# Kernel tuning notes

Measured on AMD Instinct MI355X. Metric: run time of the kernel, lower is better.

## Reference

```python
import jax, jax.numpy as jnp
import numpy as np

SL, BS, HS, FFN, E, TOPK = 2048, 4, 1024, 4096, 8, 2
T = SL * BS

def setup_inputs() -> dict:
    key = jax.random.key(0)
    k1, k2, k3, k4, k5, k6 = jax.random.split(key, 6)
    x = jax.random.normal(k1, (SL, BS, HS), dtype=jnp.float32)
    expert_weights = jax.random.uniform(k2, (T, TOPK), dtype=jnp.float32)
    expert_indices = jax.random.randint(k3, (T, TOPK), 0, E).astype(jnp.int64)
    scores = jax.random.uniform(k4, (T, TOPK), dtype=jnp.float32)
    w1 = jax.random.normal(k5, (E, HS, FFN), dtype=jnp.float32) * 0.02
    w2 = jax.random.normal(k6, (E, FFN, HS), dtype=jnp.float32) * 0.02
    return {"x": x, "expert_weights": expert_weights, "scores": scores,
            "w1": w1, "w2": w2, "expert_indices": expert_indices}

def reference(x, expert_weights, scores, w1, w2, expert_indices):
    # Dropless MoE dispatch-compute-combine with router_type=None.
    # Math identity: megablocks gather/grouped-GEMM/scatter with per-copy
    # expert_weights equals, for each token t:
    #   out[t] = sum_k expert_weights[t,k] * MLP_{e(t,k)}(x[t])
    # We fold the top-k copies into a per-(token, expert) combine weight and
    # run one GEMM pair per expert (fixed small E), matching the grouped GEMM.
    sl, bs, hs = x.shape
    num_experts = w1.shape[0]
    xf = x.reshape(-1, hs)  # [T, hs]
    onehot = jax.nn.one_hot(expert_indices, num_experts, dtype=x.dtype)  # [T, k, E]
    combine = jnp.einsum("tk,tke->et", expert_weights, onehot)  # [E, T]

    def expert_step(acc, inputs):
        w1e, w2e, cw = inputs  # [hs, ffn], [ffn, hs], [T]
        h = jax.nn.gelu(xf @ w1e, approximate=False)  # [T, ffn]
        acc = acc + cw[:, None] * (h @ w2e)  # [T, hs]
        return acc, None

    out, _ = jax.lax.scan(expert_step, jnp.zeros_like(xf), (w1, w2, combine))
    return out.reshape(sl, bs, hs)
```

## Files before the change

### kernel.cpp

```cpp
#include <hip/hip_runtime.h>
#include <hip/hip_bf16.h>
#include <math.h>
#include <stdint.h>

#define N_TOK   8192
#define HS      1024
#define FFN     4096
#define NE      8
#define NA      16384
#define CAP     16384
#define BMT     128
#define MAXT    136
#define PERMSZ  16777216ULL

typedef __attribute__((ext_vector_type(8))) short          bf16x8;
typedef __attribute__((ext_vector_type(4))) float          f32x4;
typedef __attribute__((ext_vector_type(4))) float          fvec4;
typedef __attribute__((ext_vector_type(4))) unsigned short usvec4;

__device__ __forceinline__ void gl_lds16(const void* g, void* l) {
  __builtin_amdgcn_global_load_lds(
      (const __attribute__((address_space(1))) unsigned int*)g,
      (__attribute__((address_space(3))) unsigned int*)l,
      16, 0, 0);
}

__device__ __forceinline__ unsigned short f2bf(float f) {
  union { float f; unsigned int u; } v; v.f = f;
  unsigned int r = v.u + 0x7FFFu + ((v.u >> 16) & 1u);
  return (unsigned short)(r >> 16);
}


__global__ void cvt_x_kernel(const fvec4* __restrict__ in, unsigned short* __restrict__ out, int n4) {
  int i = blockIdx.x * 256 + threadIdx.x;
  if (i >= n4) return;
  fvec4 v = in[i];
  usvec4 o;
  o[0] = f2bf(v[0]); o[1] = f2bf(v[1]); o[2] = f2bf(v[2]); o[3] = f2bf(v[3]);
  *(usvec4*)(out + (size_t)i * 4) = o;
}

__global__ void tpose_cvt_kernel(const float* __restrict__ in, unsigned short* __restrict__ out,
                                 int R, int C) {
  __shared__ float t[64][65];
  int bc = blockIdx.x * 64, br = blockIdx.y * 64, e = blockIdx.z;
  const float* ine = in + (size_t)e * R * C;
  unsigned short* oute = out + (size_t)e * R * C;
  int tx = threadIdx.x & 63, ty = threadIdx.x >> 6;
#pragma unroll
  for (int q = 0; q < 16; ++q) {
    int r = ty * 16 + q;
    t[r][tx] = ine[(size_t)(br + r) * C + bc + tx];
  }
  __syncthreads();
#pragma unroll
  for (int q = 0; q < 16; ++q) {
    int c = ty * 16 + q;
    oute[(size_t)(bc + c) * R + br + tx] = f2bf(t[tx][c]);
  }
}


__global__ void route_kernel(const int* __restrict__ idx, const float* __restrict__ wts,
                             int* __restrict__ counts, int* __restrict__ btok,
                             int* __restrict__ bslot, float* __restrict__ bw) {
  int a = blockIdx.x * 256 + threadIdx.x;
  if (a >= NA) return;
  int e = idx[a];
  int pos = atomicAdd(&counts[e], 1);
  btok[(size_t)e * CAP + pos]  = a >> 1;
  bslot[(size_t)e * CAP + pos] = a;
  bw[(size_t)e * CAP + pos]    = wts[a];
}

__global__ void build_tiles_kernel(int* __restrict__ counts, int2* __restrict__ table) {
  if (threadIdx.x == 0 && blockIdx.x == 0) {
    int nt = 0;
    for (int e = 0; e < NE; ++e) {
      int c = counts[e];
      int t = (c + BMT - 1) >> 7;
      for (int m = 0; m < t && nt < MAXT; ++m) table[nt++] = make_int2(e, m);
    }
    counts[8] = nt;
  }
}

template <int EPI, int AROW, int KTOT, int NU>
__global__ __launch_bounds__(256, 3)
void moe_gemm(const unsigned short* __restrict__ Ab,
              const unsigned short* __restrict__ Bb,
              unsigned short* __restrict__ hout,
              float* __restrict__ perm,
              const int* __restrict__ btok,
              const int* __restrict__ bslot,
              const float* __restrict__ bw,
              const int* __restrict__ counts,
              const int2* __restrict__ table,
              int* __restrict__ ctr, int p0, int tc) {
  constexpr int NT = KTOT / 32;
  __shared__ char lds[32768];
  __shared__ int s_u;

  int tid = threadIdx.x;
  int wid = tid >> 6, lane = tid & 63;
  int wm = wid >> 1, wn = wid & 1;
  int nt = counts[8];

  int rin = lane >> 2;
  int klog = ((lane & 3) * 16) ^ (((rin >> 1) & 3) << 4);
  int dst[4];
#pragma unroll
  for (int q = 0; q < 4; ++q) dst[q] = (wid * 4 + q) * 1024;

  int l15 = lane & 15, l16 = lane >> 4;
  int swzr = ((l15 >> 1) & 3) << 4;
  int ks = l16 * 16;
  int offA0 = (wm * 64 + l15) * 64 + (ks ^ swzr);
  int offB0 = 8192 + (wn * 64 + l15) * 64 + (ks ^ swzr);

  for (;;) {
    __syncthreads();
    if (tid == 0) s_u = atomicAdd(ctr, 1);
    __syncthreads();
    int u = s_u;
    if (u >= NU) return;

    int kq, col, j;
    if (EPI == 0) { kq = 0; col = u / MAXT; j = u % MAXT; }
    else          { kq = u / (8 * MAXT); int rem = u % (8 * MAXT); col = rem / MAXT; j = rem % MAXT; }
    if (j >= nt || j < p0 || j >= p0 + tc) continue;
    int2 te = table[j];
    int e = te.x, tm = te.y;
    int count = counts[e];
    int slotb = j - p0;
    int bn0 = col * 128;
    int kbyte0 = kq * (KTOT * 2);

    const unsigned short* Be = Bb + (size_t)e * ((size_t)FFN * HS);

    const char* src[4];
#pragma unroll
    for (int q = 0; q < 4; ++q) {
      int c = wid * 4 + q;
      if (c < 8) {
        int row = c * 16 + rin;
        if (EPI == 0) {
          int grow = tm * BMT + row;
          int tok = (grow < count) ? btok[(size_t)e * CAP + grow] : 0;
          src[q] = (const char*)(Ab + (size_t)tok * AROW) + kbyte0 + klog;
        } else {
          src[q] = (const char*)(Ab + ((size_t)slotb * BMT + row) * AROW) + kbyte0 + klog;
        }
      } else {
        int nrow = bn0 + (c - 8) * 16 + rin;
        src[q] = (const char*)(Be + (size_t)nrow * AROW) + kbyte0 + klog;
      }
    }

    f32x4 acc[4][4] = {};

#pragma unroll
    for (int q = 0; q < 4; ++q) gl_lds16(src[q], lds + dst[q]);
    asm volatile("s_waitcnt vmcnt(0)" ::: "memory");
    __builtin_amdgcn_s_barrier();
    __builtin_amdgcn_sched_barrier(0);

    for (int t = 0; t < NT; ++t) {
      const char* rbuf = lds + (t & 1) * 16384;
      char* db = lds + ((t + 1) & 1) * 16384;
      if (t + 1 < NT) {
#pragma unroll
        for (int q = 0; q < 4; ++q)
          gl_lds16(src[q] + (size_t)(t + 1) * 64, db + dst[q]);
      }
      bf16x8 a[4], b[4];
#pragma unroll
      for (int n = 0; n < 4; ++n) b[n] = *(const bf16x8*)(rbuf + offB0 + n * 1024);
#pragma unroll
      for (int i = 0; i < 4; ++i) a[i] = *(const bf16x8*)(rbuf + offA0 + i * 1024);
      __builtin_amdgcn_s_setprio(1);
#pragma unroll
      for (int i = 0; i < 4; ++i)
#pragma unroll
        for (int n = 0; n < 4; ++n)
          acc[i][n] = __builtin_amdgcn_mfma_f32_16x16x32_bf16(a[i], b[n], acc[i][n], 0, 0, 0);
      __builtin_amdgcn_s_setprio(0);
      __builtin_amdgcn_sched_barrier(0);
      asm volatile("s_waitcnt vmcnt(0)" ::: "memory");
      __builtin_amdgcn_s_barrier();
      __builtin_amdgcn_sched_barrier(0);
    }

    char* wlds = lds + wid * 8192;
#pragma unroll
    for (int p = 0; p < 2; ++p) {
#pragma unroll
      for (int ii = 0; ii < 2; ++ii) {
        int i = p * 2 + ii;
#pragma unroll
        for (int n = 0; n < 4; ++n) {
          int waddr = (ii * 16 + l16 * 4) * 256 + (n * 16 + l15) * 4;
#pragma unroll
          for (int rr = 0; rr < 4; ++rr)
            *(float*)(wlds + waddr + rr * 256) = acc[i][n][rr];
        }
      }
      asm volatile("s_waitcnt lgkmcnt(0)" ::: "memory");
      __builtin_amdgcn_sched_barrier(0);
#pragma unroll
      for (int rd = 0; rd < 8; ++rd) {
        int row = rd * 4 + l16;
        f32x4 v = *(const f32x4*)(wlds + row * 256 + l15 * 16);
        int colg = bn0 + wn * 64 + l15 * 4;
        if (EPI == 0) {
          usvec4 o;
#pragma unroll
          for (int z = 0; z < 4; ++z) {
            float vv = v[z];
            float x2 = vv * vv;
            float u2 = 1.5957691216057308f * vv * fmaf(0.044715f, x2, 1.0f);
            u2 = fminf(fmaxf(u2, -30.f), 30.f);
            float ee = __expf(u2);
            o[z] = f2bf(vv * __fdividef(ee, ee + 1.0f));
          }
          size_t hrow = (size_t)slotb * BMT + wm * 64 + p * 32 + row;
          *(usvec4*)(hout + hrow * FFN + colg) = o;
        } else {
          int grow = tm * BMT + wm * 64 + p * 32 + row;
          if (grow < count) {
            int s = bslot[(size_t)e * CAP + grow];
            float wgt = bw[(size_t)e * CAP + grow];
            fvec4 o;
#pragma unroll
            for (int z = 0; z < 4; ++z) o[z] = wgt * v[z];
            *(fvec4*)(perm + (size_t)kq * PERMSZ + (size_t)s * HS + colg) = o;
          }
        }
      }
      __builtin_amdgcn_sched_barrier(0);
    }
  }
}

__global__ void combine_kernel(const fvec4* __restrict__ perm, fvec4* __restrict__ out, int n4) {
  int i = blockIdx.x * 256 + threadIdx.x;
  if (i >= n4) return;
  int t = i >> 8;
  int c = i & 255;
  const fvec4* p0 = perm;
  const fvec4* p1 = perm + PERMSZ / 4;
  size_t r0 = (size_t)(2 * t) * 256 + c;
  size_t r1 = (size_t)(2 * t + 1) * 256 + c;
  out[i] = (p0[r0] + p1[r0]) + (p0[r1] + p1[r1]);
}


extern "C" void kernel_launch(void* const* d_in, const int* in_sizes, int n_in,
                              void* d_out, int out_size, void* d_ws, size_t ws_size,
                              hipStream_t stream) {
  const float* x   = (const float*)d_in[0];
  const float* ew  = (const float*)d_in[1];
  const float* w1  = (const float*)d_in[3];
  const float* w2  = (const float*)d_in[4];
  const int*   eix = (const int*)d_in[5];

  char* ws = (char*)d_ws;
  const size_t o_w1T    = 0;
  const size_t o_w2T    = 67108864ULL;
  const size_t o_xb     = 134217728ULL;
  const size_t o_btok   = 150994944ULL;
  const size_t o_bslot  = 151519232ULL;
  const size_t o_bw     = 152043520ULL;
  const size_t o_counts = 152567808ULL;
  const size_t o_table  = 152568064ULL;
  const size_t o_ctr    = 152570112ULL;
  const size_t o_perm   = 152572160ULL;
  const size_t o_h      = 286789888ULL;

  unsigned short* w1T = (unsigned short*)(ws + o_w1T);
  unsigned short* w2T = (unsigned short*)(ws + o_w2T);
  unsigned short* xb  = (unsigned short*)(ws + o_xb);
  int*   btok   = (int*)(ws + o_btok);
  int*   bslot  = (int*)(ws + o_bslot);
  float* bw     = (float*)(ws + o_bw);
  int*   counts = (int*)(ws + o_counts);
  int2*  table  = (int2*)(ws + o_table);
  int*   ctrs   = (int*)(ws + o_ctr);
  float* perm   = (float*)(ws + o_perm);
  unsigned short* hbuf = (unsigned short*)(ws + o_h);

  long long havail = (long long)ws_size - (long long)o_h;
  long long tile_bytes = (long long)BMT * FFN * 2;
  int tc = (int)(havail / tile_bytes);
  if (tc < 1) tc = 1;
  if (tc > MAXT) tc = MAXT;
  int npass = (MAXT + tc - 1) / tc;
  if (npass > 128) npass = 128;

  hipMemsetAsync(counts, 0, 256, stream);
  hipMemsetAsync(ctrs, 0, 2048, stream);

  cvt_x_kernel<<<(N_TOK * HS / 4 + 255) / 256, 256, 0, stream>>>(
      (const fvec4*)x, xb, N_TOK * HS / 4);
  tpose_cvt_kernel<<<dim3(FFN / 64, HS / 64, NE), 256, 0, stream>>>(w1, w1T, HS, FFN);
  tpose_cvt_kernel<<<dim3(HS / 64, FFN / 64, NE), 256, 0, stream>>>(w2, w2T, FFN, HS);

  route_kernel<<<(NA + 255) / 256, 256, 0, stream>>>(eix, ew, counts, btok, bslot, bw);
  build_tiles_kernel<<<1, 64, 0, stream>>>(counts, table);

  for (int p = 0; p < npass; ++p) {
    moe_gemm<0, HS, HS, 32 * MAXT><<<dim3(1024), 256, 0, stream>>>(
        xb, w1T, hbuf, perm, btok, bslot, bw, counts, table,
        &ctrs[p * 2 + 0], p * tc, tc);
    moe_gemm<1, FFN, FFN / 2, 2 * 8 * MAXT><<<dim3(1024), 256, 0, stream>>>(
        hbuf, w2T, hbuf, perm, btok, bslot, bw, counts, table,
        &ctrs[p * 2 + 1], p * tc, tc);
  }

  combine_kernel<<<(N_TOK * HS / 4 + 255) / 256, 256, 0, stream>>>(
      (const fvec4*)perm, (fvec4*)d_out, N_TOK * HS / 4);
}
```

Baseline: 684.1 us.

## Use 256x256 GEMM tiles with pre-packed swizzled operands and 4-stage LDS pipeline

Doubles the M tile to 256 rows and the N tile to 256 columns with 512-thread blocks and 128KB of LDS. The weights, the gathered tokens and the hidden activations are stored in a pre-tiled, swizzled bf16 layout, so each operand chunk is one contiguous 16KB block. Token gathering and conversion move into a separate pack kernel that runs after routing. The K loop becomes a 4-buffer ring with 3 stages in flight, replacing the previous double buffer with a full vmcnt(0) drain every step. This aims to raise operand reuse and hide memory latency, at the cost of 1 block per CU, more padding waste per expert from 256-row tiles, and a larger workspace.

Result: slower. 795.4 us (+16.3%).

```diff
diff --git a/kernel.cpp b/kernel.cpp
--- a/kernel.cpp
+++ b/kernel.cpp
@@ -9,14 +9,15 @@
 #define NE      8
 #define NA      16384
 #define CAP     16384
-#define BMT     128
-#define MAXT    136
+#define BMT     256
+#define MAXT    72
 #define PERMSZ  16777216ULL
 
 typedef __attribute__((ext_vector_type(8))) short          bf16x8;
 typedef __attribute__((ext_vector_type(4))) float          f32x4;
 typedef __attribute__((ext_vector_type(4))) float          fvec4;
 typedef __attribute__((ext_vector_type(4))) unsigned short usvec4;
+typedef __attribute__((ext_vector_type(8))) unsigned short usvec8;
 
 __device__ __forceinline__ void gl_lds16(const void* g, void* l) {
   __builtin_amdgcn_global_load_lds(
@@ -29,36 +30,6 @@
   union { float f; unsigned int u; } v; v.f = f;
   unsigned int r = v.u + 0x7FFFu + ((v.u >> 16) & 1u);
   return (unsigned short)(r >> 16);
-}
-
-
-__global__ void cvt_x_kernel(const fvec4* __restrict__ in, unsigned short* __restrict__ out, int n4) {
-  int i = blockIdx.x * 256 + threadIdx.x;
-  if (i >= n4) return;
-  fvec4 v = in[i];
-  usvec4 o;
-  o[0] = f2bf(v[0]); o[1] = f2bf(v[1]); o[2] = f2bf(v[2]); o[3] = f2bf(v[3]);
-  *(usvec4*)(out + (size_t)i * 4) = o;
-}
-
-__global__ void tpose_cvt_kernel(const float* __restrict__ in, unsigned short* __restrict__ out,
-                                 int R, int C) {
-  __shared__ float t[64][65];
-  int bc = blockIdx.x * 64, br = blockIdx.y * 64, e = blockIdx.z;
-  const float* ine = in + (size_t)e * R * C;
-  unsigned short* oute = out + (size_t)e * R * C;
-  int tx = threadIdx.x & 63, ty = threadIdx.x >> 6;
-#pragma unroll
-  for (int q = 0; q < 16; ++q) {
-    int r = ty * 16 + q;
-    t[r][tx] = ine[(size_t)(br + r) * C + bc + tx];
-  }
-  __syncthreads();
-#pragma unroll
-  for (int q = 0; q < 16; ++q) {
-    int c = ty * 16 + q;
-    oute[(size_t)(bc + c) * R + br + tx] = f2bf(t[tx][c]);
-  }
 }
 
 
@@ -79,122 +50,163 @@
     int nt = 0;
     for (int e = 0; e < NE; ++e) {
       int c = counts[e];
-      int t = (c + BMT - 1) >> 7;
+      int t = (c + BMT - 1) >> 8;
       for (int m = 0; m < t && nt < MAXT; ++m) table[nt++] = make_int2(e, m);
     }
     counts[8] = nt;
   }
 }
 
-template <int EPI, int AROW, int KTOT, int NU>
-__global__ __launch_bounds__(256, 3)
-void moe_gemm(const unsigned short* __restrict__ Ab,
-              const unsigned short* __restrict__ Bb,
+
+__global__ void pack_x_kernel(const float* __restrict__ x,
+                              unsigned short* __restrict__ xg,
+                              const int* __restrict__ btok,
+                              const int* __restrict__ counts,
+                              const int2* __restrict__ table) {
+  int j = blockIdx.x, kt = blockIdx.y, row = threadIdx.x;
+  int nt = counts[8];
+  if (j >= nt) return;
+  int2 te = table[j];
+  int e = te.x, tm = te.y;
+  int count = counts[e];
+  int grow = tm * BMT + row;
+  int tok = (grow < count) ? btok[(size_t)e * CAP + grow] : 0;
+  const fvec4* src = (const fvec4*)(x + (size_t)tok * HS + kt * 32);
+  char* dst = (char*)xg + ((size_t)j * 32 + kt) * 16384 + row * 64;
+  int swz = (row >> 1) & 3;
+#pragma unroll
+  for (int s = 0; s < 4; ++s) {
+    fvec4 v0 = src[2 * s], v1 = src[2 * s + 1];
+    usvec8 o;
+    o[0] = f2bf(v0[0]); o[1] = f2bf(v0[1]); o[2] = f2bf(v0[2]); o[3] = f2bf(v0[3]);
+    o[4] = f2bf(v1[0]); o[5] = f2bf(v1[1]); o[6] = f2bf(v1[2]); o[7] = f2bf(v1[3]);
+    *(usvec8*)(dst + ((s ^ swz) << 4)) = o;
+  }
+}
+
+__global__ void pack_w_kernel(const float* __restrict__ in, unsigned short* __restrict__ out,
+                              int R, int C) {
+  __shared__ float t[64][65];
+  int bc = blockIdx.x * 64, br = blockIdx.y * 64, e = blockIdx.z;
+  const float* ine = in + (size_t)e * R * C;
+  char* oute = (char*)out + (size_t)e * R * C * 2;
+  int tx = threadIdx.x & 63, ty = threadIdx.x >> 6;
+#pragma unroll
+  for (int q = 0; q < 16; ++q) {
+    int r = ty * 16 + q;
+    t[r][tx] = ine[(size_t)(br + r) * C + bc + tx];
+  }
+  __syncthreads();
+  int nkt = R / 32;
+#pragma unroll
+  for (int q = 0; q < 16; ++q) {
+    int c = ty * 16 + q;
+    int n = bc + c, k = br + tx;
+    size_t addr = (((size_t)(n >> 8) * nkt + (k >> 5)) * 256 + (n & 255)) * 64
+                + ((size_t)((((k & 31) >> 3) ^ ((n >> 1) & 3)) << 4)) + (k & 7) * 2;
+    *(unsigned short*)(oute + addr) = f2bf(t[tx][c]);
+  }
+}
+
+template <int EPI, int NKT, int NUNIT>
+__global__ __launch_bounds__(512, 1)
+void moe_gemm(const unsigned short* __restrict__ Apk,
+              const unsigned short* __restrict__ Bpk,
               unsigned short* __restrict__ hout,
               float* __restrict__ perm,
-              const int* __restrict__ btok,
               const int* __restrict__ bslot,
               const float* __restrict__ bw,
               const int* __restrict__ counts,
               const int2* __restrict__ table,
               int* __restrict__ ctr, int p0, int tc) {
-  constexpr int NT = KTOT / 32;
-  __shared__ char lds[32768];
+  __shared__ char lds[131072];
   __shared__ int s_u;
 
-  int tid = threadIdx.x;
-  int wid = tid >> 6, lane = tid & 63;
-  int wm = wid >> 1, wn = wid & 1;
+  int tid = threadIdx.x, wid = tid >> 6, lane = tid & 63;
+  int wm = wid >> 2, wn = wid & 3;
+  int l15 = lane & 15, l16 = lane >> 4;
   int nt = counts[8];
 
-  int rin = lane >> 2;
-  int klog = ((lane & 3) * 16) ^ (((rin >> 1) & 3) << 4);
-  int dst[4];
-#pragma unroll
-  for (int q = 0; q < 4; ++q) dst[q] = (wid * 4 + q) * 1024;
-
-  int l15 = lane & 15, l16 = lane >> 4;
-  int swzr = ((l15 >> 1) & 3) << 4;
-  int ks = l16 * 16;
-  int offA0 = (wm * 64 + l15) * 64 + (ks ^ swzr);
-  int offB0 = 8192 + (wn * 64 + l15) * 64 + (ks ^ swzr);
+  int swz16 = (l16 ^ ((l15 >> 1) & 3)) << 4;
+  int offA0 = (wm * 128 + l15) * 64 + swz16;
+  int offB0 = 16384 + (wn * 64 + l15) * 64 + swz16;
+  int cbase[4];
+#pragma unroll
+  for (int q = 0; q < 4; ++q) cbase[q] = (wid * 4 + q) * 1024;
 
   for (;;) {
     __syncthreads();
     if (tid == 0) s_u = atomicAdd(ctr, 1);
     __syncthreads();
     int u = s_u;
-    if (u >= NU) return;
-
-    int kq, col, j;
-    if (EPI == 0) { kq = 0; col = u / MAXT; j = u % MAXT; }
-    else          { kq = u / (8 * MAXT); int rem = u % (8 * MAXT); col = rem / MAXT; j = rem % MAXT; }
+    if (u >= NUNIT) return;
+
+    int j, col, kq;
+    if (EPI == 0) { col = u / MAXT; j = u - col * MAXT; kq = 0; }
+    else { int g = u / MAXT; j = u - g * MAXT; col = g & 3; kq = g >> 2; }
     if (j >= nt || j < p0 || j >= p0 + tc) continue;
     int2 te = table[j];
     int e = te.x, tm = te.y;
     int count = counts[e];
     int slotb = j - p0;
-    int bn0 = col * 128;
-    int kbyte0 = kq * (KTOT * 2);
-
-    const unsigned short* Be = Bb + (size_t)e * ((size_t)FFN * HS);
-
-    const char* src[4];
+
+    const char* Asrc; const char* Bsrc;
+    if (EPI == 0) {
+      Asrc = (const char*)Apk + (size_t)j * (32 * 16384);
+      Bsrc = (const char*)Bpk + (size_t)e * 8388608 + (size_t)col * (32 * 16384);
+    } else {
+      Asrc = (const char*)Apk + (size_t)slotb * (128 * 16384) + (size_t)kq * (64 * 16384);
+      Bsrc = (const char*)Bpk + (size_t)e * 8388608 + (size_t)col * (128 * 16384)
+           + (size_t)kq * (64 * 16384);
+    }
+    const char* csrc[4];
 #pragma unroll
     for (int q = 0; q < 4; ++q) {
       int c = wid * 4 + q;
-      if (c < 8) {
-        int row = c * 16 + rin;
-        if (EPI == 0) {
-          int grow = tm * BMT + row;
-          int tok = (grow < count) ? btok[(size_t)e * CAP + grow] : 0;
-          src[q] = (const char*)(Ab + (size_t)tok * AROW) + kbyte0 + klog;
-        } else {
-          src[q] = (const char*)(Ab + ((size_t)slotb * BMT + row) * AROW) + kbyte0 + klog;
-        }
-      } else {
-        int nrow = bn0 + (c - 8) * 16 + rin;
-        src[q] = (const char*)(Be + (size_t)nrow * AROW) + kbyte0 + klog;
-      }
-    }
-
-    f32x4 acc[4][4] = {};
-
-#pragma unroll
-    for (int q = 0; q < 4; ++q) gl_lds16(src[q], lds + dst[q]);
-    asm volatile("s_waitcnt vmcnt(0)" ::: "memory");
-    __builtin_amdgcn_s_barrier();
-    __builtin_amdgcn_sched_barrier(0);
-
-    for (int t = 0; t < NT; ++t) {
-      const char* rbuf = lds + (t & 1) * 16384;
-      char* db = lds + ((t + 1) & 1) * 16384;
-      if (t + 1 < NT) {
-#pragma unroll
-        for (int q = 0; q < 4; ++q)
-          gl_lds16(src[q] + (size_t)(t + 1) * 64, db + dst[q]);
-      }
-      bf16x8 a[4], b[4];
+      csrc[q] = (c < 16 ? Asrc + c * 1024 : Bsrc + (c - 16) * 1024) + lane * 16;
+    }
+
+    f32x4 acc[8][4] = {};
+
+#pragma unroll
+    for (int s = 0; s < 3; ++s)
+#pragma unroll
+      for (int q = 0; q < 4; ++q)
+        gl_lds16(csrc[q] + (size_t)s * 16384, lds + s * 32768 + cbase[q]);
+
+    for (int hk = 0; hk < NKT; ++hk) {
+      asm volatile("s_waitcnt vmcnt(8)" ::: "memory");
+      __builtin_amdgcn_sched_barrier(0);
+      __builtin_amdgcn_s_barrier();
+      __builtin_amdgcn_sched_barrier(0);
+
+      int hs = hk + 3; if (hs >= NKT) hs -= NKT;
+      char* db = lds + (hs & 3) * 32768;
+#pragma unroll
+      for (int q = 0; q < 4; ++q)
+        gl_lds16(csrc[q] + (size_t)hs * 16384, db + cbase[q]);
+
+      const char* rbuf = lds + (hk & 3) * 32768;
+      bf16x8 a[8], b[4];
 #pragma unroll
       for (int n = 0; n < 4; ++n) b[n] = *(const bf16x8*)(rbuf + offB0 + n * 1024);
 #pragma unroll
-      for (int i = 0; i < 4; ++i) a[i] = *(const bf16x8*)(rbuf + offA0 + i * 1024);
+      for (int i = 0; i < 8; ++i) a[i] = *(const bf16x8*)(rbuf + offA0 + i * 1024);
       __builtin_amdgcn_s_setprio(1);
 #pragma unroll
-      for (int i = 0; i < 4; ++i)
+      for (int i = 0; i < 8; ++i)
 #pragma unroll
         for (int n = 0; n < 4; ++n)
           acc[i][n] = __builtin_amdgcn_mfma_f32_16x16x32_bf16(a[i], b[n], acc[i][n], 0, 0, 0);
       __builtin_amdgcn_s_setprio(0);
       __builtin_amdgcn_sched_barrier(0);
-      asm volatile("s_waitcnt vmcnt(0)" ::: "memory");
-      __builtin_amdgcn_s_barrier();
-      __builtin_amdgcn_sched_barrier(0);
-    }
+    }
+    asm volatile("s_waitcnt vmcnt(0)" ::: "memory");
+    __builtin_amdgcn_s_barrier();
 
     char* wlds = lds + wid * 8192;
 #pragma unroll
-    for (int p = 0; p < 2; ++p) {
+    for (int p = 0; p < 4; ++p) {
 #pragma unroll
       for (int ii = 0; ii < 2; ++ii) {
         int i = p * 2 + ii;
@@ -212,7 +224,8 @@
       for (int rd = 0; rd < 8; ++rd) {
         int row = rd * 4 + l16;
         f32x4 v = *(const f32x4*)(wlds + row * 256 + l15 * 16);
-        int colg = bn0 + wn * 64 + l15 * 4;
+        int colg = col * 256 + wn * 64 + l15 * 4;
+        int hrow = wm * 128 + p * 32 + row;
         if (EPI == 0) {
           usvec4 o;
 #pragma unroll
@@ -224,10 +237,13 @@
             float ee = __expf(u2);
             o[z] = f2bf(vv * __fdividef(ee, ee + 1.0f));
           }
-          size_t hrow = (size_t)slotb * BMT + wm * 64 + p * 32 + row;
-          *(usvec4*)(hout + hrow * FFN + colg) = o;
+          int kt = colg >> 5;
+          int slotc = ((colg & 31) >> 3) ^ ((hrow >> 1) & 3);
+          char* hpc = (char*)hout + (size_t)slotb * 2097152 + (size_t)kt * 16384
+                    + hrow * 64 + (slotc << 4) + (colg & 7) * 2;
+          *(usvec4*)hpc = o;
         } else {
-          int grow = tm * BMT + wm * 64 + p * 32 + row;
+          int grow = tm * BMT + hrow;
           if (grow < count) {
             int s = bslot[(size_t)e * CAP + grow];
             float wgt = bw[(size_t)e * CAP + grow];
@@ -266,21 +282,21 @@
   const int*   eix = (const int*)d_in[5];
 
   char* ws = (char*)d_ws;
-  const size_t o_w1T    = 0;
-  const size_t o_w2T    = 67108864ULL;
-  const size_t o_xb     = 134217728ULL;
-  const size_t o_btok   = 150994944ULL;
-  const size_t o_bslot  = 151519232ULL;
-  const size_t o_bw     = 152043520ULL;
-  const size_t o_counts = 152567808ULL;
-  const size_t o_table  = 152568064ULL;
-  const size_t o_ctr    = 152570112ULL;
-  const size_t o_perm   = 152572160ULL;
-  const size_t o_h      = 286789888ULL;
-
-  unsigned short* w1T = (unsigned short*)(ws + o_w1T);
-  unsigned short* w2T = (unsigned short*)(ws + o_w2T);
-  unsigned short* xb  = (unsigned short*)(ws + o_xb);
+  const size_t o_w1p    = 0;
+  const size_t o_w2p    = 67108864ULL;
+  const size_t o_xg     = 134217728ULL;
+  const size_t o_btok   = 171966464ULL;
+  const size_t o_bslot  = 172490752ULL;
+  const size_t o_bw     = 173015040ULL;
+  const size_t o_counts = 173539328ULL;
+  const size_t o_table  = 173539584ULL;
+  const size_t o_ctr    = 173541632ULL;
+  const size_t o_perm   = 173543680ULL;
+  const size_t o_hp     = 307761408ULL;
+
+  unsigned short* w1p = (unsigned short*)(ws + o_w1p);
+  unsigned short* w2p = (unsigned short*)(ws + o_w2p);
+  unsigned short* xg  = (unsigned short*)(ws + o_xg);
   int*   btok   = (int*)(ws + o_btok);
   int*   bslot  = (int*)(ws + o_bslot);
   float* bw     = (float*)(ws + o_bw);
@@ -288,11 +304,10 @@
   int2*  table  = (int2*)(ws + o_table);
   int*   ctrs   = (int*)(ws + o_ctr);
   float* perm   = (float*)(ws + o_perm);
-  unsigned short* hbuf = (unsigned short*)(ws + o_h);
-
-  long long havail = (long long)ws_size - (long long)o_h;
-  long long tile_bytes = (long long)BMT * FFN * 2;
-  int tc = (int)(havail / tile_bytes);
+  unsigned short* hp = (unsigned short*)(ws + o_hp);
+
+  long long havail = (long long)ws_size - (long long)o_hp;
+  int tc = (int)(havail / 2097152LL);
   if (tc < 1) tc = 1;
   if (tc > MAXT) tc = MAXT;
   int npass = (MAXT + tc - 1) / tc;
@@ -301,21 +316,18 @@
   hipMemsetAsync(counts, 0, 256, stream);
   hipMemsetAsync(ctrs, 0, 2048, stream);
 
-  cvt_x_kernel<<<(N_TOK * HS / 4 + 255) / 256, 256, 0, stream>>>(
-      (const fvec4*)x, xb, N_TOK * HS / 4);
-  tpose_cvt_kernel<<<dim3(FFN / 64, HS / 64, NE), 256, 0, stream>>>(w1, w1T, HS, FFN);
-  tpose_cvt_kernel<<<dim3(HS / 64, FFN / 64, NE), 256, 0, stream>>>(w2, w2T, FFN, HS);
-
   route_kernel<<<(NA + 255) / 256, 256, 0, stream>>>(eix, ew, counts, btok, bslot, bw);
   build_tiles_kernel<<<1, 64, 0, stream>>>(counts, table);
 
+  pack_x_kernel<<<dim3(MAXT, 32), 256, 0, stream>>>(x, xg, btok, counts, table);
+  pack_w_kernel<<<dim3(FFN / 64, HS / 64, NE), 256, 0, stream>>>(w1, w1p, HS, FFN);
+  pack_w_kernel<<<dim3(HS / 64, FFN / 64, NE), 256, 0, stream>>>(w2, w2p, FFN, HS);
+
   for (int p = 0; p < npass; ++p) {
-    moe_gemm<0, HS, HS, 32 * MAXT><<<dim3(1024), 256, 0, stream>>>(
-        xb, w1T, hbuf, perm, btok, bslot, bw, counts, table,
-        &ctrs[p * 2 + 0], p * tc, tc);
-    moe_gemm<1, FFN, FFN / 2, 2 * 8 * MAXT><<<dim3(1024), 256, 0, stream>>>(
-        hbuf, w2T, hbuf, perm, btok, bslot, bw, counts, table,
-        &ctrs[p * 2 + 1], p * tc, tc);
+    moe_gemm<0, 32, 16 * MAXT><<<dim3(256), 512, 0, stream>>>(
+        xg, w1p, hp, perm, bslot, bw, counts, table, &ctrs[p * 2 + 0], p * tc, tc);
+    moe_gemm<1, 64, 8 * MAXT><<<dim3(256), 512, 0, stream>>>(
+        hp, w2p, hp, perm, bslot, bw, counts, table, &ctrs[p * 2 + 1], p * tc, tc);
   }
 
   combine_kernel<<<(N_TOK * HS / 4 + 255) / 256, 256, 0, stream>>>(
```
